# Performance work log

Hardware: AMD Instinct MI355X
Metric: run time of the kernel (lower is better)

## Reference

```python
import jax, jax.numpy as jnp
import numpy as np

N, E, T = 6144, 98304, 32
D_IN, D, D_FF, H, OUT = 128, 256, 256, 4, 2
DH = D // H
EPS = 1e-5


def setup_inputs() -> dict:
    key = jax.random.key(0)
    ks = jax.random.split(key, 24)
    s = 0.05
    inp = {
        "x": jax.random.normal(ks[0], (N, D_IN), jnp.float32),
        "edge_index": jax.random.randint(ks[1], (2, E), 0, N, jnp.int64 if jax.config.jax_enable_x64 else jnp.int32),
        "timesteps": jnp.sort(jax.random.randint(ks[2], (N,), 0, T)),
        "lin_l_w": jax.random.normal(ks[3], (D, D_IN), jnp.float32) * s,
        "lin_l_b": jnp.zeros((D,), jnp.float32),
        "lin_r_w": jax.random.normal(ks[4], (D, D_IN), jnp.float32) * s,
        "bn_gamma": jnp.ones((D,), jnp.float32),
        "bn_beta": jnp.zeros((D,), jnp.float32),
        "in_proj_w": jax.random.normal(ks[5], (2, 3 * D, D), jnp.float32) * s,
        "in_proj_b": jnp.zeros((2, 3 * D), jnp.float32),
        "out_w": jax.random.normal(ks[6], (2, D, D), jnp.float32) * s,
        "out_b": jnp.zeros((2, D), jnp.float32),
        "ff1_w": jax.random.normal(ks[7], (2, D_FF, D), jnp.float32) * s,
        "ff1_b": jnp.zeros((2, D_FF), jnp.float32),
        "ff2_w": jax.random.normal(ks[8], (2, D, D_FF), jnp.float32) * s,
        "ff2_b": jnp.zeros((2, D), jnp.float32),
        "ln1_g": jnp.ones((2, D), jnp.float32),
        "ln1_b": jnp.zeros((2, D), jnp.float32),
        "ln2_g": jnp.ones((2, D), jnp.float32),
        "ln2_b": jnp.zeros((2, D), jnp.float32),
        "cls_w": jax.random.normal(ks[9], (OUT, D), jnp.float32) * s,
        "cls_b": jnp.zeros((OUT,), jnp.float32),
    }
    return inp


def _layernorm(h, g, b):
    mu = jnp.mean(h, -1, keepdims=True)
    v = jnp.var(h, -1, keepdims=True)
    return (h - mu) * jax.lax.rsqrt(v + EPS) * g + b


def _forward(x, edge_index, timesteps, lin_l_w, lin_l_b, lin_r_w, bn_gamma, bn_beta,
             in_proj_w, in_proj_b, out_w, out_b, ff1_w, ff1_b, ff2_w, ff2_b,
             ln1_g, ln1_b, ln2_g, ln2_b, cls_w, cls_b):
    # SAGEConv (mean aggregation): out = lin_l(mean_{j->i} x_j) + lin_r(x_i)
    src, dst = edge_index[0], edge_index[1]
    agg = jax.ops.segment_sum(x[src], dst, num_segments=N)
    cnt = jax.ops.segment_sum(jnp.ones((E,), x.dtype), dst, num_segments=N)
    agg = agg / jnp.maximum(cnt, 1.0)[:, None]
    h = agg @ lin_l_w.T + lin_l_b + x @ lin_r_w.T

    # BatchNorm1d (training batch stats) + ReLU
    mu = jnp.mean(h, 0)
    var = jnp.var(h, 0)
    h = (h - mu) * jax.lax.rsqrt(var + EPS) * bn_gamma + bn_beta
    h = jax.nn.relu(h)

    # Per-timestep transformer == full attention with block-diagonal mask
    mask = timesteps[:, None] == timesteps[None, :]  # [N, N]
    neg = jnp.finfo(h.dtype).min

    for l in range(2):
        # self-attention (post-norm TransformerEncoderLayer)
        qkv = h @ in_proj_w[l].T + in_proj_b[l]             # [N, 3D]
        q, k, v = jnp.split(qkv, 3, axis=-1)
        q = q.reshape(N, H, DH).transpose(1, 0, 2)          # [H, N, DH]
        k = k.reshape(N, H, DH).transpose(1, 0, 2)
        v = v.reshape(N, H, DH).transpose(1, 0, 2)
        scores = jnp.einsum('hnd,hmd->hnm', q, k) / jnp.sqrt(jnp.asarray(DH, h.dtype))
        scores = jnp.where(mask[None], scores, neg)
        attn = jax.nn.softmax(scores, axis=-1)
        o = jnp.einsum('hnm,hmd->hnd', attn, v).transpose(1, 0, 2).reshape(N, D)
        o = o @ out_w[l].T + out_b[l]
        h = _layernorm(h + o, ln1_g[l], ln1_b[l])
        # FFN
        f = jax.nn.relu(h @ ff1_w[l].T + ff1_b[l]) @ ff2_w[l].T + ff2_b[l]
        h = _layernorm(h + f, ln2_g[l], ln2_b[l])

    return h @ cls_w.T + cls_b  # [N, OUT]


def reference(x, edge_index, timesteps, lin_l_w, lin_l_b, lin_r_w, bn_gamma, bn_beta,
              in_proj_w, in_proj_b, out_w, out_b, ff1_w, ff1_b, ff2_w, ff2_b,
              ln1_g, ln1_b, ln2_g, ln2_b, cls_w, cls_b):
    return _forward(x, edge_index, timesteps, lin_l_w, lin_l_b, lin_r_w, bn_gamma, bn_beta,
                    in_proj_w, in_proj_b, out_w, out_b, ff1_w, ff1_b, ff2_w, ff2_b,
                    ln1_g, ln1_b, ln2_g, ln2_b, cls_w, cls_b)
```

## Files before the change

kernel.cpp:

```cpp
#include <hip/hip_runtime.h>

#define NN   6144
#define EE   98304
#define DIN  128
#define DD   256
#define TT   32
#define NH   4
#define ATTN_Z 6
#define WROWS 3328

typedef __attribute__((ext_vector_type(8))) short short8;
typedef __attribute__((ext_vector_type(4))) float f32x4;
typedef unsigned short u16;

__device__ __forceinline__ float bf2f(u16 u) {
    return __uint_as_float(((unsigned)u) << 16);
}
__device__ __forceinline__ u16 f2bf(float f) {
    unsigned u = __float_as_uint(f);
    return (u16)((u + 0x7fffu + ((u >> 16) & 1u)) >> 16);
}
__device__ __forceinline__ unsigned pk2(float a, float b) {
    return (unsigned)f2bf(a) | ((unsigned)f2bf(b) << 16);
}
__device__ __forceinline__ float bnrelu(float v, float s, float q, float g, float b) {
    float mu = s * (1.0f / NN);
    float var = q * (1.0f / NN) - mu * mu;
    return fmaxf((v - mu) * rsqrtf(var + 1e-5f) * g + b, 0.0f);
}

__global__ void aml_hist_k(const int* __restrict__ ei, int* __restrict__ deg) {
    int e = blockIdx.x * 256 + threadIdx.x;
    if (e < EE) atomicAdd(&deg[ei[EE + e]], 1);
}

__global__ void aml_scan_k(const int* __restrict__ deg, int* __restrict__ rowptr,
                           int* __restrict__ cursor) {
    int t = threadIdx.x;
    int base = t * 24;
    int loc[24];
    int s = 0;
    #pragma unroll
    for (int j = 0; j < 24; ++j) { loc[j] = s; s += deg[base + j]; }
    __shared__ int part[256];
    part[t] = s;
    __syncthreads();
    for (int o = 1; o < 256; o <<= 1) {
        int v = (t >= o) ? part[t - o] : 0;
        __syncthreads();
        part[t] += v;
        __syncthreads();
    }
    int off = (t > 0) ? part[t - 1] : 0;
    #pragma unroll
    for (int j = 0; j < 24; ++j) {
        rowptr[base + j] = off + loc[j];
        cursor[base + j] = off + loc[j];
    }
    if (t == 255) rowptr[NN] = part[255];
}

__global__ void aml_scatter2_k(const int* __restrict__ ei, int* __restrict__ cursor,
                               int* __restrict__ eid) {
    int e = blockIdx.x * 256 + threadIdx.x;
    if (e >= EE) return;
    int slot = atomicAdd(&cursor[ei[EE + e]], 1);
    eid[slot] = ei[e];
}

__global__ void aml_gather_k(const float* __restrict__ x, const int* __restrict__ rowptr,
                             const int* __restrict__ eid, u16* __restrict__ ac) {
    int node = blockIdx.x * 4 + (threadIdx.x >> 6);
    int lane = threadIdx.x & 63;
    int p0 = rowptr[node], p1 = rowptr[node + 1];
    float ax = 0.f, ay = 0.f;
    int j = p0;
    for (; j + 1 < p1; j += 2) {
        int s0 = eid[j], s1 = eid[j + 1];
        float2 v0 = *(const float2*)(x + (size_t)s0 * DIN + lane * 2);
        float2 v1 = *(const float2*)(x + (size_t)s1 * DIN + lane * 2);
        ax += v0.x + v1.x; ay += v0.y + v1.y;
    }
    if (j < p1) {
        float2 v = *(const float2*)(x + (size_t)eid[j] * DIN + lane * 2);
        ax += v.x; ay += v.y;
    }
    float inv = 1.0f / fmaxf((float)(p1 - p0), 1.0f);
    float2 xr = *(const float2*)(x + (size_t)node * DIN + lane * 2);
    *(unsigned*)(ac + (size_t)node * DD + lane * 2) = pk2(ax * inv, ay * inv);
    *(unsigned*)(ac + (size_t)node * DD + DIN + lane * 2) = pk2(xr.x, xr.y);
}

__global__ void aml_prep_k(const float* __restrict__ lin_l_w, const float* __restrict__ lin_r_w,
                           const float* __restrict__ inp_w, const float* __restrict__ out_w,
                           const float* __restrict__ ff1_w, const float* __restrict__ ff2_w,
                           const int* __restrict__ ts, u16* __restrict__ wb,
                           int* __restrict__ offs, float* __restrict__ zero_region) {
    int r = blockIdx.x;
    if (r > WROWS) {
        zero_region[(r - WROWS - 1) * 256 + threadIdx.x] = 0.0f;
        return;
    }
    if (r == WROWS) {
        int t = threadIdx.x;
        if (t <= TT) {
            int lo = 0, hi = NN;
            while (lo < hi) { int mid = (lo + hi) >> 1; if (ts[mid] < t) lo = mid + 1; else hi = mid; }
            offs[t] = lo;
        }
        return;
    }
    int k = threadIdx.x;
    float v;
    if (r < 256) {
        v = (k < DIN) ? lin_l_w[r * DIN + k] : lin_r_w[r * DIN + (k - DIN)];
    } else {
        int r2 = r - 256;
        int l = r2 / 1536, r3 = r2 % 1536;
        const float* src; int rr;
        if (r3 < 768)       { src = inp_w + (size_t)l * 768 * DD; rr = r3; }
        else if (r3 < 1024) { src = out_w + (size_t)l * DD * DD;  rr = r3 - 768; }
        else if (r3 < 1280) { src = ff1_w + (size_t)l * DD * DD;  rr = r3 - 1024; }
        else                { src = ff2_w + (size_t)l * DD * DD;  rr = r3 - 1280; }
        v = src[(size_t)rr * DD + k];
    }
    wb[(size_t)r * DD + k] = f2bf(v);
}

template <int RELU, int AMODE, int CF32, int BNSTAT, int CT2>
__global__ __launch_bounds__(256)
void aml_gemm_k(const void* __restrict__ A, const u16* __restrict__ Wb,
                const float* __restrict__ bias, void* __restrict__ C, int M,
                float* __restrict__ stats, const float* __restrict__ bng,
                const float* __restrict__ bnb, float* __restrict__ h2) {
    __shared__ __align__(16) unsigned char lds[65536];
    const int t = threadIdx.x;
    const int brow = blockIdx.x * 64;
    const int bcol = blockIdx.y * (64 * CT2);

    #pragma unroll
    for (int p = 0; p < 8; ++p) {
        int c = t + p * 256;
        int row = c >> 5;
        int colb = (c & 31) * 16;
        int dst = row * 512 + (colb ^ ((row & 7) << 4));
        if (AMODE == 2) {
            int d0 = (c & 31) * 8;
            const u16* sA = (const u16*)A + (size_t)(brow + row) * 256 + d0;
            uint4 raw = *(const uint4*)sA;
            const u16* rp = (const u16*)&raw;
            float av[8];
            #pragma unroll
            for (int i = 0; i < 8; ++i) {
                int d = d0 + i;
                av[i] = bnrelu(bf2f(rp[i]), stats[d], stats[DD + d], bng[d], bnb[d]);
            }
            if (blockIdx.y == 0) {
                float* hp = h2 + (size_t)(brow + row) * 256 + d0;
                *(float4*)hp = make_float4(av[0], av[1], av[2], av[3]);
                *(float4*)(hp + 4) = make_float4(av[4], av[5], av[6], av[7]);
            }
            uint4 pa = { pk2(av[0], av[1]), pk2(av[2], av[3]), pk2(av[4], av[5]), pk2(av[6], av[7]) };
            *(uint4*)(lds + dst) = pa;
        } else {
            const u16* sA = (const u16*)A + (size_t)(brow + row) * 256 + (c & 31) * 8;
            *(uint4*)(lds + dst) = *(const uint4*)sA;
        }
        *(uint4*)(lds + 32768 + dst) =
            *(const uint4*)(Wb + (size_t)(bcol + row) * 256 + (c & 31) * 8);
    }
    __syncthreads();

    const int wave = t >> 6, lane = t & 63;
    const int lrow = lane & 15, lk = lane >> 4;
    const int arow = wave * 16 + lrow;

    short8 af[8];
    #pragma unroll
    for (int ks = 0; ks < 8; ++ks) {
        int kbyte = ks * 64 + lk * 16;
        af[ks] = *(const short8*)(lds + arow * 512 + (kbyte ^ ((arow & 7) << 4)));
    }

    f32x4 acc[CT2][4] = {};
    #pragma unroll
    for (int c2 = 0; c2 < CT2; ++c2) {
        if (c2) {
            __syncthreads();
            #pragma unroll
            for (int p = 0; p < 8; ++p) {
                int c = t + p * 256;
                int row = c >> 5;
                int colb = (c & 31) * 16;
                int dst = 32768 + row * 512 + (colb ^ ((row & 7) << 4));
                *(uint4*)(lds + dst) =
                    *(const uint4*)(Wb + (size_t)(bcol + c2 * 64 + row) * 256 + (c & 31) * 8);
            }
            __syncthreads();
        }
        #pragma unroll
        for (int ks = 0; ks < 8; ++ks) {
            int kbyte = ks * 64 + lk * 16;
            #pragma unroll
            for (int ct = 0; ct < 4; ++ct) {
                int wrow = ct * 16 + lrow;
                short8 bf = *(const short8*)(lds + 32768 + wrow * 512 + (kbyte ^ ((wrow & 7) << 4)));
                acc[c2][ct] = __builtin_amdgcn_mfma_f32_16x16x32_bf16(af[ks], bf, acc[c2][ct], 0, 0, 0);
            }
        }
    }

    #pragma unroll
    for (int c2 = 0; c2 < CT2; ++c2) {
        #pragma unroll
        for (int ct = 0; ct < 4; ++ct) {
            int col = bcol + c2 * 64 + ct * 16 + lrow;
            float bv = bias[col];
            float s = 0.f, q = 0.f;
            #pragma unroll
            for (int r = 0; r < 4; ++r) {
                int grow = brow + wave * 16 + lk * 4 + r;
                float v = acc[c2][ct][r] + bv;
                if (RELU) v = fmaxf(v, 0.0f);
                if (CF32) ((float*)C)[(size_t)grow * M + col] = v;
                else      ((u16*)C)[(size_t)grow * M + col] = f2bf(v);
                if (BNSTAT) { s += v; q += v * v; }
            }
            if (BNSTAT) {
                s += __shfl_xor(s, 16); s += __shfl_xor(s, 32);
                q += __shfl_xor(q, 16); q += __shfl_xor(q, 32);
                if (lk == 0) {
                    atomicAdd(&stats[col], s);
                    atomicAdd(&stats[DD + col], q);
                }
            }
        }
    }
}

#define TAIL_GEMM(WPTR, LOADA)                                                            \
    _Pragma("unroll")                                                                     \
    for (int kc = 0; kc < 4; ++kc) {                                                      \
        __syncthreads();                                                                  \
        _Pragma("unroll")                                                                 \
        for (int p = 0; p < 8; ++p) {                                                     \
            int c = t + p * 256;                                                          \
            int row = c >> 3, sub = c & 7;                                                \
            *(uint4*)(Wl + row * 128 + ((sub * 16) ^ ((row & 7) << 4))) =                 \
                *(const uint4*)((WPTR) + (size_t)row * 256 + kc * 64 + sub * 8);          \
        }                                                                                 \
        __syncthreads();                                                                  \
        if ((LOADA) && kc == 0) {                                                         \
            _Pragma("unroll")                                                             \
            for (int ks = 0; ks < 8; ++ks) {                                              \
                int kbyte = ks * 64 + lk * 16;                                            \
                af[ks] = *(const short8*)(Al + lrow * 512 + (kbyte ^ ((lrow & 7) << 4))); \
            }                                                                             \
        }                                                                                 \
        _Pragma("unroll")                                                                 \
        for (int s = 0; s < 2; ++s) {                                                     \
            int kb = s * 64 + lk * 16;                                                    \
            _Pragma("unroll")                                                             \
            for (int ct = 0; ct < 4; ++ct) {                                              \
                int wrow = wcol + ct * 16 + lrow;                                         \
                short8 bf = *(const short8*)(Wl + wrow * 128 + (kb ^ ((wrow & 7) << 4))); \
                acc[ct] = __builtin_amdgcn_mfma_f32_16x16x32_bf16(af[kc * 2 + s], bf,     \
                                                                  acc[ct], 0, 0, 0);      \
            }                                                                             \
        }                                                                                 \
    }

#define WRITE_AL(VARR)                                                                    \
    _Pragma("unroll")                                                                     \
    for (int ct = 0; ct < 4; ++ct) {                                                      \
        _Pragma("unroll")                                                                 \
        for (int r = 0; r < 4; ++r) {                                                     \
            int row = lk * 4 + r, col = wcol + ct * 16 + lrow;                            \
            *(u16*)(Al + row * 512 + ((col * 2) ^ ((row & 7) << 4))) = f2bf(VARR[ct][r]); \
        }                                                                                 \
    }

#define ROW_LN_STATS(S4, Q4, MU, IV)                                                      \
    _Pragma("unroll")                                                                     \
    for (int off = 1; off < 16; off <<= 1) {                                              \
        _Pragma("unroll")                                                                 \
        for (int r = 0; r < 4; ++r) {                                                     \
            S4[r] += __shfl_xor(S4[r], off);                                              \
            Q4[r] += __shfl_xor(Q4[r], off);                                              \
        }                                                                                 \
    }                                                                                     \
    if (lrow == 0) {                                                                      \
        _Pragma("unroll")                                                                 \
        for (int r = 0; r < 4; ++r) {                                                     \
            reds[wave][lk * 4 + r] = S4[r];                                               \
            redq[wave][lk * 4 + r] = Q4[r];                                               \
        }                                                                                 \
    }                                                                                     \
    __syncthreads();                                                                      \
    _Pragma("unroll")                                                                     \
    for (int r = 0; r < 4; ++r) {                                                         \
        int rr = lk * 4 + r;                                                              \
        float S = reds[0][rr] + reds[1][rr] + reds[2][rr] + reds[3][rr];                  \
        float Q = redq[0][rr] + redq[1][rr] + redq[2][rr] + redq[3][rr];                  \
        MU[r] = S * (1.0f / DD);                                                          \
        IV[r] = rsqrtf(Q * (1.0f / DD) - MU[r] * MU[r] + 1e-5f);                          \
    }

template <int LAST>
__global__ __launch_bounds__(256)
void aml_tail_k(const u16* __restrict__ A, float* __restrict__ h2,
                const u16* __restrict__ Wout, const float* __restrict__ bout,
                const float* __restrict__ g1, const float* __restrict__ b1,
                const u16* __restrict__ Wff1, const float* __restrict__ bff1,
                const u16* __restrict__ Wff2, const float* __restrict__ bff2,
                const float* __restrict__ g2, const float* __restrict__ b2,
                const u16* __restrict__ Wq, const float* __restrict__ bq,
                u16* __restrict__ qkv,
                const float* __restrict__ cls_w, const float* __restrict__ cls_b,
                float* __restrict__ out) {
    __shared__ __align__(16) unsigned char Al[8192];
    __shared__ __align__(16) unsigned char Wl[32768];
    __shared__ float reds[4][16], redq[4][16];
    __shared__ float redc[2][4][16];
    const int t = threadIdx.x;
    const int brow = blockIdx.x * 16;
    const int wave = t >> 6, lane = t & 63;
    const int lrow = lane & 15, lk = lane >> 4;
    const int wcol = wave * 64;

    #pragma unroll
    for (int p = 0; p < 2; ++p) {
        int c = t + p * 256;
        int row = c >> 5, c8 = c & 31;
        *(uint4*)(Al + row * 512 + ((c8 * 16) ^ ((row & 7) << 4))) =
            *(const uint4*)(A + (size_t)(brow + row) * 256 + c8 * 8);
    }

    short8 af[8];
    f32x4 acc[4];

    #pragma unroll
    for (int ct = 0; ct < 4; ++ct) acc[ct] = (f32x4){0.f, 0.f, 0.f, 0.f};
    TAIL_GEMM(Wout, true)

    float ln1v[4][4];
    {
        float s4[4] = {}, q4[4] = {};
        #pragma unroll
        for (int ct = 0; ct < 4; ++ct) {
            int col = wcol + ct * 16 + lrow;
            float bvv = bout[col];
            #pragma unroll
            for (int r = 0; r < 4; ++r) {
                int grow = brow + lk * 4 + r;
                float v = acc[ct][r] + bvv + h2[(size_t)grow * DD + col];
                acc[ct][r] = v;
                s4[r] += v; q4[r] += v * v;
            }
        }
        float mu[4], iv[4];
        ROW_LN_STATS(s4, q4, mu, iv)
        #pragma unroll
        for (int ct = 0; ct < 4; ++ct) {
            int col = wcol + ct * 16 + lrow;
            float gv = g1[col], bb = b1[col];
            #pragma unroll
            for (int r = 0; r < 4; ++r)
                ln1v[ct][r] = (acc[ct][r] - mu[r]) * iv[r] * gv + bb;
        }
        WRITE_AL(ln1v)
    }

    #pragma unroll
    for (int ct = 0; ct < 4; ++ct) acc[ct] = (f32x4){0.f, 0.f, 0.f, 0.f};
    TAIL_GEMM(Wff1, true)
    {
        float fv[4][4];
        #pragma unroll
        for (int ct = 0; ct < 4; ++ct) {
            int col = wcol + ct * 16 + lrow;
            float bvv = bff1[col];
            #pragma unroll
            for (int r = 0; r < 4; ++r)
                fv[ct][r] = fmaxf(acc[ct][r] + bvv, 0.0f);
        }
        __syncthreads();
        WRITE_AL(fv)
    }

    #pragma unroll
    for (int ct = 0; ct < 4; ++ct) acc[ct] = (f32x4){0.f, 0.f, 0.f, 0.f};
    TAIL_GEMM(Wff2, true)
    float ln2v[4][4];
    {
        float s4[4] = {}, q4[4] = {};
        #pragma unroll
        for (int ct = 0; ct < 4; ++ct) {
            int col = wcol + ct * 16 + lrow;
            float bvv = bff2[col];
            #pragma unroll
            for (int r = 0; r < 4; ++r) {
                float v = acc[ct][r] + bvv + ln1v[ct][r];
                acc[ct][r] = v;
                s4[r] += v; q4[r] += v * v;
            }
        }
        float mu[4], iv[4];
        ROW_LN_STATS(s4, q4, mu, iv)
        #pragma unroll
        for (int ct = 0; ct < 4; ++ct) {
            int col = wcol + ct * 16 + lrow;
            float gv = g2[col], bb = b2[col];
            #pragma unroll
            for (int r = 0; r < 4; ++r) {
                float v = (acc[ct][r] - mu[r]) * iv[r] * gv + bb;
                ln2v[ct][r] = v;
                if (!LAST) {
                    int grow = brow + lk * 4 + r;
                    h2[(size_t)grow * DD + col] = v;
                }
            }
        }
        if (!LAST) {
            WRITE_AL(ln2v)
        }
    }

    if (!LAST) {
        #pragma unroll
        for (int cg = 0; cg < 3; ++cg) {
            #pragma unroll
            for (int ct = 0; ct < 4; ++ct) acc[ct] = (f32x4){0.f, 0.f, 0.f, 0.f};
            TAIL_GEMM(Wq + (size_t)cg * 256 * 256, cg == 0)
            #pragma unroll
            for (int ct = 0; ct < 4; ++ct) {
                int col = cg * 256 + wcol + ct * 16 + lrow;
                float bvv = bq[col];
                #pragma unroll
                for (int r = 0; r < 4; ++r) {
                    int grow = brow + lk * 4 + r;
                    qkv[(size_t)grow * 768 + col] = f2bf(acc[ct][r] + bvv);
                }
            }
        }
    } else {
        float c0[4] = {}, c1[4] = {};
        #pragma unroll
        for (int ct = 0; ct < 4; ++ct) {
            int col = wcol + ct * 16 + lrow;
            float w0 = cls_w[col], w1 = cls_w[DD + col];
            #pragma unroll
            for (int r = 0; r < 4; ++r) {
                c0[r] += ln2v[ct][r] * w0;
                c1[r] += ln2v[ct][r] * w1;
            }
        }
        #pragma unroll
        for (int off = 1; off < 16; off <<= 1) {
            #pragma unroll
            for (int r = 0; r < 4; ++r) {
                c0[r] += __shfl_xor(c0[r], off);
                c1[r] += __shfl_xor(c1[r], off);
            }
        }
        if (lrow == 0) {
            #pragma unroll
            for (int r = 0; r < 4; ++r) {
                redc[0][wave][lk * 4 + r] = c0[r];
                redc[1][wave][lk * 4 + r] = c1[r];
            }
        }
        __syncthreads();
        if (wave == 0 && lrow == 0) {
            float cb0 = cls_b[0], cb1 = cls_b[1];
            #pragma unroll
            for (int r = 0; r < 4; ++r) {
                int rr = lk * 4 + r;
                float o0 = redc[0][0][rr] + redc[0][1][rr] + redc[0][2][rr] + redc[0][3][rr];
                float o1 = redc[1][0][rr] + redc[1][1][rr] + redc[1][2][rr] + redc[1][3][rr];
                out[(brow + rr) * 2]     = o0 + cb0;
                out[(brow + rr) * 2 + 1] = o1 + cb1;
            }
        }
    }
}

__global__ __launch_bounds__(256)
void aml_attn_k(const u16* __restrict__ qkv, const int* __restrict__ offs,
                u16* __restrict__ o) {
    int tb = blockIdx.x, head = blockIdx.y, z = blockIdx.z;
    int start = offs[tb], end = offs[tb + 1];
    int S = end - start;
    if (S <= z * 64) return;
    int t = threadIdx.x, wave = t >> 6, lane = t & 63;
    int lq = lane & 15, lk = lane >> 4;
    int qoff = head * 64;

    __shared__ __align__(16) unsigned char Kl[8192];
    __shared__ __align__(16) unsigned char Vt[8192];
    __shared__ __align__(16) unsigned char Pl[4][2048];
    __shared__ float Ol[4][16][65];

    int qi = start + z * 64 + wave * 16 + lq;
    int qic = min(qi, end - 1);
    const u16* qp = qkv + (size_t)qic * 768 + qoff + lk * 8;
    short8 qf[2];
    qf[0] = *(const short8*)qp;
    qf[1] = *(const short8*)(qp + 32);

    float m = -1e30f, l = 0.f;
    f32x4 acc[4] = {};

    int ntile = (S + 63) >> 6;
    for (int tile = 0; tile < ntile; ++tile) {
        int jcnt = S - tile * 64; if (jcnt > 64) jcnt = 64;
        {
            int j = t >> 2, d0 = (t & 3) * 16;
            unsigned char* krow = Kl + j * 128;
            if (j < jcnt) {
                const u16* kp = qkv + (size_t)(start + tile * 64 + j) * 768 + 256 + qoff + d0;
                *(uint4*)(krow + ((d0 * 2) ^ ((j & 7) << 4))) = *(const uint4*)kp;
                *(uint4*)(krow + ((d0 * 2 + 16) ^ ((j & 7) << 4))) = *(const uint4*)(kp + 8);
            } else {
                uint4 zz = { 0, 0, 0, 0 };
                *(uint4*)(krow + ((d0 * 2) ^ ((j & 7) << 4))) = zz;
                *(uint4*)(krow + ((d0 * 2 + 16) ^ ((j & 7) << 4))) = zz;
            }
        }
        {
            int j0 = (t & 31) * 2, d0v = (t >> 5) * 8;
            const u16* vbase = qkv + (size_t)(start + tile * 64) * 768 + 512 + qoff + d0v;
            uint4 va = { 0, 0, 0, 0 }, vb = { 0, 0, 0, 0 };
            if (j0 < jcnt)     va = *(const uint4*)(vbase + (size_t)j0 * 768);
            if (j0 + 1 < jcnt) vb = *(const uint4*)(vbase + (size_t)(j0 + 1) * 768);
            const u16* pa = (const u16*)&va;
            const u16* pb = (const u16*)&vb;
            #pragma unroll
            for (int i = 0; i < 8; ++i) {
                int d = d0v + i;
                unsigned w = (unsigned)pa[i] | ((unsigned)pb[i] << 16);
                *(unsigned*)(Vt + d * 128 + ((j0 * 2) ^ ((d & 7) << 4))) = w;
            }
        }
        __syncthreads();

        f32x4 sv[4];
        #pragma unroll
        for (int kt = 0; kt < 4; ++kt) {
            int kr = kt * 16 + lq;
            f32x4 s = {};
            #pragma unroll
            for (int ks = 0; ks < 2; ++ks) {
                short8 kf = *(const short8*)(Kl + kr * 128 + ((ks * 64 + lk * 16) ^ ((kr & 7) << 4)));
                s = __builtin_amdgcn_mfma_f32_16x16x32_bf16(kf, qf[ks], s, 0, 0, 0);
            }
            sv[kt] = s;
        }
        float pm = -1e30f;
        #pragma unroll
        for (int kt = 0; kt < 4; ++kt) {
            #pragma unroll
            for (int r = 0; r < 4; ++r) {
                int kk = tile * 64 + kt * 16 + lk * 4 + r;
                float s = (kk < S) ? sv[kt][r] * 0.125f : -1e30f;
                sv[kt][r] = s;
                pm = fmaxf(pm, s);
            }
        }
        pm = fmaxf(pm, __shfl_xor(pm, 16));
        pm = fmaxf(pm, __shfl_xor(pm, 32));
        float mn = fmaxf(m, pm);
        float corr = __expf(m - mn);
        m = mn;
        float ps = 0.f;
        #pragma unroll
        for (int kt = 0; kt < 4; ++kt) {
            #pragma unroll
            for (int r = 0; r < 4; ++r) {
                float p = __expf(sv[kt][r] - mn);
                sv[kt][r] = p;
                ps += p;
            }
            uint2 w = { pk2(sv[kt][0], sv[kt][1]), pk2(sv[kt][2], sv[kt][3]) };
            *(uint2*)(Pl[wave] + lq * 128 + ((kt * 32 + lk * 8) ^ ((lq & 7) << 4))) = w;
        }
        ps += __shfl_xor(ps, 16);
        ps += __shfl_xor(ps, 32);
        l = l * corr + ps;
        #pragma unroll
        for (int dt = 0; dt < 4; ++dt) {
            #pragma unroll
            for (int r = 0; r < 4; ++r) acc[dt][r] *= corr;
        }
        #pragma unroll
        for (int ks = 0; ks < 2; ++ks) {
            short8 pf = *(const short8*)(Pl[wave] + lq * 128 + ((ks * 64 + lk * 16) ^ ((lq & 7) << 4)));
            #pragma unroll
            for (int dt = 0; dt < 4; ++dt) {
                int dr = dt * 16 + lq;
                short8 vf = *(const short8*)(Vt + dr * 128 + ((ks * 64 + lk * 16) ^ ((dr & 7) << 4)));
                acc[dt] = __builtin_amdgcn_mfma_f32_16x16x32_bf16(vf, pf, acc[dt], 0, 0, 0);
            }
        }
        __syncthreads();
    }

    float linv = 1.0f / l;
    #pragma unroll
    for (int dt = 0; dt < 4; ++dt) {
        #pragma unroll
        for (int r = 0; r < 4; ++r)
            Ol[wave][lq][dt * 16 + lk * 4 + r] = acc[dt][r] * linv;
    }
    int q2 = lane >> 2, c2 = lane & 3;
    int qg = start + z * 64 + wave * 16 + q2;
    if (qg < end) {
        u16* op = o + (size_t)qg * DD + qoff + c2 * 16;
        const float* sp = &Ol[wave][q2][c2 * 16];
        #pragma unroll
        for (int i = 0; i < 8; ++i)
            ((unsigned*)op)[i] = pk2(sp[2 * i], sp[2 * i + 1]);
    }
}

extern "C" void kernel_launch(void* const* d_in, const int* in_sizes, int n_in,
                              void* d_out, int out_size, void* d_ws, size_t ws_size,
                              hipStream_t stream) {
    const float* x       = (const float*)d_in[0];
    const int*   ei      = (const int*)d_in[1];
    const int*   ts      = (const int*)d_in[2];
    const float* lin_l_w = (const float*)d_in[3];
    const float* lin_l_b = (const float*)d_in[4];
    const float* lin_r_w = (const float*)d_in[5];
    const float* bn_g    = (const float*)d_in[6];
    const float* bn_b    = (const float*)d_in[7];
    const float* inp_w   = (const float*)d_in[8];
    const float* inp_b   = (const float*)d_in[9];
    const float* out_w   = (const float*)d_in[10];
    const float* out_b   = (const float*)d_in[11];
    const float* ff1_w   = (const float*)d_in[12];
    const float* ff1_b   = (const float*)d_in[13];
    const float* ff2_w   = (const float*)d_in[14];
    const float* ff2_b   = (const float*)d_in[15];
    const float* ln1_g   = (const float*)d_in[16];
    const float* ln1_b   = (const float*)d_in[17];
    const float* ln2_g   = (const float*)d_in[18];
    const float* ln2_b   = (const float*)d_in[19];
    const float* cls_w   = (const float*)d_in[20];
    const float* cls_b   = (const float*)d_in[21];

    float* ws     = (float*)d_ws;
    float* stats  = ws;
    int*   deg    = (int*)(stats + 512);
    int*   rowptr = deg + NN;
    int*   cursor = rowptr + NN + 4;
    int*   eid    = cursor + NN;
    int*   offs   = eid + EE;
    u16*   wb     = (u16*)(offs + 64);
    u16*   hb     = wb + (size_t)WROWS * 256;
    float* h2     = (float*)(hb + (size_t)NN * DD);
    u16*   qkv    = (u16*)(h2 + (size_t)NN * DD);
    u16*   t1     = qkv + (size_t)NN * 768;
    u16*   ac     = qkv;

    const u16* wb_cat = wb;
    const u16* wb_inp[2] = { wb + (size_t)(256) * 256,        wb + (size_t)(256 + 1536) * 256 };
    const u16* wb_out[2] = { wb + (size_t)(256 + 768) * 256,  wb + (size_t)(256 + 1536 + 768) * 256 };
    const u16* wb_ff1[2] = { wb + (size_t)(256 + 1024) * 256, wb + (size_t)(256 + 1536 + 1024) * 256 };
    const u16* wb_ff2[2] = { wb + (size_t)(256 + 1280) * 256, wb + (size_t)(256 + 1536 + 1280) * 256 };

    aml_prep_k<<<WROWS + 27, 256, 0, stream>>>(lin_l_w, lin_r_w, inp_w, out_w, ff1_w, ff2_w,
                                               ts, wb, offs, stats);
    aml_hist_k<<<EE / 256, 256, 0, stream>>>(ei, deg);
    aml_scan_k<<<1, 256, 0, stream>>>(deg, rowptr, cursor);
    aml_scatter2_k<<<EE / 256, 256, 0, stream>>>(ei, cursor, eid);
    aml_gather_k<<<NN / 4, 256, 0, stream>>>(x, rowptr, eid, ac);
    aml_gemm_k<0, 0, 0, 1, 1><<<dim3(NN / 64, 4), 256, 0, stream>>>(
        ac, wb_cat, lin_l_b, hb, DD, stats, nullptr, nullptr, nullptr);
    aml_gemm_k<0, 2, 0, 0, 1><<<dim3(NN / 64, 12), 256, 0, stream>>>(
        hb, wb_inp[0], inp_b, qkv, 768, stats, bn_g, bn_b, h2);

    aml_attn_k<<<dim3(TT, NH, ATTN_Z), 256, 0, stream>>>(qkv, offs, t1);
    aml_tail_k<0><<<NN / 16, 256, 0, stream>>>(
        t1, h2, wb_out[0], out_b, ln1_g, ln1_b,
        wb_ff1[0], ff1_b, wb_ff2[0], ff2_b, ln2_g, ln2_b,
        wb_inp[1], inp_b + 768, qkv, nullptr, nullptr, nullptr);

    aml_attn_k<<<dim3(TT, NH, ATTN_Z), 256, 0, stream>>>(qkv, offs, t1);
    aml_tail_k<1><<<NN / 16, 256, 0, stream>>>(
        t1, h2, wb_out[1], out_b + DD, ln1_g + DD, ln1_b + DD,
        wb_ff1[1], ff1_b + DD, wb_ff2[1], ff2_b + DD, ln2_g + DD, ln2_b + DD,
        nullptr, nullptr, nullptr, cls_w, cls_b, (float*)d_out);
}
```

Measured before the change: 153.8 us.

## Split attention over key tiles with a separate log-sum-exp combine kernel

Each attention block now handles one 64-query by 64-key tile pair instead of looping over all key tiles. It writes unnormalized fp32 partial outputs plus per-row max and sum to workspace. A new combine kernel merges the partials per query with the usual rescaling and writes the bf16 output. The aim is more parallel blocks and shorter serial loops per block. The cost is extra fp32 partial traffic to global memory and one more launch per layer.

```diff
diff --git a/kernel.cpp b/kernel.cpp
--- a/kernel.cpp
+++ b/kernel.cpp
@@ -6,7 +6,8 @@
 #define DD   256
 #define TT   32
 #define NH   4
-#define ATTN_Z 6
+#define ZQ   6
+#define ZK   6
 #define WROWS 3328
 
 typedef __attribute__((ext_vector_type(8))) short short8;
@@ -487,11 +488,13 @@
 
 __global__ __launch_bounds__(256)
 void aml_attn_k(const u16* __restrict__ qkv, const int* __restrict__ offs,
-                u16* __restrict__ o) {
-    int tb = blockIdx.x, head = blockIdx.y, z = blockIdx.z;
+                float* __restrict__ Opart, float* __restrict__ mpart,
+                float* __restrict__ lpart) {
+    int tb = blockIdx.x, head = blockIdx.y;
+    int zq = blockIdx.z / ZK, zk = blockIdx.z % ZK;
     int start = offs[tb], end = offs[tb + 1];
     int S = end - start;
-    if (S <= z * 64) return;
+    if (S <= zq * 64 || zk * 64 >= S) return;
     int t = threadIdx.x, wave = t >> 6, lane = t & 63;
     int lq = lane & 15, lk = lane >> 4;
     int qoff = head * 64;
@@ -501,126 +504,147 @@
     __shared__ __align__(16) unsigned char Pl[4][2048];
     __shared__ float Ol[4][16][65];
 
-    int qi = start + z * 64 + wave * 16 + lq;
+    int qi = start + zq * 64 + wave * 16 + lq;
     int qic = min(qi, end - 1);
     const u16* qp = qkv + (size_t)qic * 768 + qoff + lk * 8;
     short8 qf[2];
     qf[0] = *(const short8*)qp;
     qf[1] = *(const short8*)(qp + 32);
 
-    float m = -1e30f, l = 0.f;
+    int jcnt = S - zk * 64; if (jcnt > 64) jcnt = 64;
+    {
+        int j = t >> 2, d0 = (t & 3) * 16;
+        unsigned char* krow = Kl + j * 128;
+        if (j < jcnt) {
+            const u16* kp = qkv + (size_t)(start + zk * 64 + j) * 768 + 256 + qoff + d0;
+            *(uint4*)(krow + ((d0 * 2) ^ ((j & 7) << 4))) = *(const uint4*)kp;
+            *(uint4*)(krow + ((d0 * 2 + 16) ^ ((j & 7) << 4))) = *(const uint4*)(kp + 8);
+        } else {
+            uint4 zz = { 0, 0, 0, 0 };
+            *(uint4*)(krow + ((d0 * 2) ^ ((j & 7) << 4))) = zz;
+            *(uint4*)(krow + ((d0 * 2 + 16) ^ ((j & 7) << 4))) = zz;
+        }
+    }
+    {
+        int j0 = (t & 31) * 2, d0v = (t >> 5) * 8;
+        const u16* vbase = qkv + (size_t)(start + zk * 64) * 768 + 512 + qoff + d0v;
+        uint4 va = { 0, 0, 0, 0 }, vb = { 0, 0, 0, 0 };
+        if (j0 < jcnt)     va = *(const uint4*)(vbase + (size_t)j0 * 768);
+        if (j0 + 1 < jcnt) vb = *(const uint4*)(vbase + (size_t)(j0 + 1) * 768);
+        const u16* pa = (const u16*)&va;
+        const u16* pb = (const u16*)&vb;
+        #pragma unroll
+        for (int i = 0; i < 8; ++i) {
+            int d = d0v + i;
+            unsigned w = (unsigned)pa[i] | ((unsigned)pb[i] << 16);
+            *(unsigned*)(Vt + d * 128 + ((j0 * 2) ^ ((d & 7) << 4))) = w;
+        }
+    }
+    __syncthreads();
+
+    f32x4 sv[4];
+    #pragma unroll
+    for (int kt = 0; kt < 4; ++kt) {
+        int kr = kt * 16 + lq;
+        f32x4 s = {};
+        #pragma unroll
+        for (int ks = 0; ks < 2; ++ks) {
+            short8 kf = *(const short8*)(Kl + kr * 128 + ((ks * 64 + lk * 16) ^ ((kr & 7) << 4)));
+            s = __builtin_amdgcn_mfma_f32_16x16x32_bf16(kf, qf[ks], s, 0, 0, 0);
+        }
+        sv[kt] = s;
+    }
+    float pm = -1e30f;
+    #pragma unroll
+    for (int kt = 0; kt < 4; ++kt) {
+        #pragma unroll
+        for (int r = 0; r < 4; ++r) {
+            int kk = zk * 64 + kt * 16 + lk * 4 + r;
+            float s = (kk < S) ? sv[kt][r] * 0.125f : -1e30f;
+            sv[kt][r] = s;
+            pm = fmaxf(pm, s);
+        }
+    }
+    pm = fmaxf(pm, __shfl_xor(pm, 16));
+    pm = fmaxf(pm, __shfl_xor(pm, 32));
+    float ps = 0.f;
+    #pragma unroll
+    for (int kt = 0; kt < 4; ++kt) {
+        #pragma unroll
+        for (int r = 0; r < 4; ++r) {
+            float p = __expf(sv[kt][r] - pm);
+            sv[kt][r] = p;
+            ps += p;
+        }
+        uint2 w = { pk2(sv[kt][0], sv[kt][1]), pk2(sv[kt][2], sv[kt][3]) };
+        *(uint2*)(Pl[wave] + lq * 128 + ((kt * 32 + lk * 8) ^ ((lq & 7) << 4))) = w;
+    }
+    ps += __shfl_xor(ps, 16);
+    ps += __shfl_xor(ps, 32);
+    if (lk == 0 && qi < end) {
+        mpart[((size_t)zk * NN + qi) * NH + head] = pm;
+        lpart[((size_t)zk * NN + qi) * NH + head] = ps;
+    }
     f32x4 acc[4] = {};
-
+    #pragma unroll
+    for (int ks = 0; ks < 2; ++ks) {
+        short8 pf = *(const short8*)(Pl[wave] + lq * 128 + ((ks * 64 + lk * 16) ^ ((lq & 7) << 4)));
+        #pragma unroll
+        for (int dt = 0; dt < 4; ++dt) {
+            int dr = dt * 16 + lq;
+            short8 vf = *(const short8*)(Vt + dr * 128 + ((ks * 64 + lk * 16) ^ ((dr & 7) << 4)));
+            acc[dt] = __builtin_amdgcn_mfma_f32_16x16x32_bf16(vf, pf, acc[dt], 0, 0, 0);
+        }
+    }
+
+    #pragma unroll
+    for (int dt = 0; dt < 4; ++dt) {
+        #pragma unroll
+        for (int r = 0; r < 4; ++r)
+            Ol[wave][lq][dt * 16 + lk * 4 + r] = acc[dt][r];
+    }
+    int q2 = lane >> 2, c2 = lane & 3;
+    int qg = start + zq * 64 + wave * 16 + q2;
+    if (qg < end) {
+        float* op = Opart + ((size_t)zk * NN + qg) * DD + qoff + c2 * 16;
+        const float* sp = &Ol[wave][q2][c2 * 16];
+        #pragma unroll
+        for (int i = 0; i < 4; ++i) ((float4*)op)[i] = *(const float4*)(sp + i * 4);
+    }
+}
+
+__global__ __launch_bounds__(256)
+void aml_comb_k(const float* __restrict__ Opart, const float* __restrict__ mpart,
+                const float* __restrict__ lpart, const int* __restrict__ ts,
+                const int* __restrict__ offs, u16* __restrict__ o) {
+    int t = threadIdx.x, head = t >> 6, lane = t & 63;
+    int lq = lane & 15, ld = lane >> 4;
+    int q = blockIdx.x * 16 + lq;
+    int tb = ts[q];
+    int S = offs[tb + 1] - offs[tb];
     int ntile = (S + 63) >> 6;
-    for (int tile = 0; tile < ntile; ++tile) {
-        int jcnt = S - tile * 64; if (jcnt > 64) jcnt = 64;
-        {
-            int j = t >> 2, d0 = (t & 3) * 16;
-            unsigned char* krow = Kl + j * 128;
-            if (j < jcnt) {
-                const u16* kp = qkv + (size_t)(start + tile * 64 + j) * 768 + 256 + qoff + d0;
-                *(uint4*)(krow + ((d0 * 2) ^ ((j & 7) << 4))) = *(const uint4*)kp;
-                *(uint4*)(krow + ((d0 * 2 + 16) ^ ((j & 7) << 4))) = *(const uint4*)(kp + 8);
-            } else {
-                uint4 zz = { 0, 0, 0, 0 };
-                *(uint4*)(krow + ((d0 * 2) ^ ((j & 7) << 4))) = zz;
-                *(uint4*)(krow + ((d0 * 2 + 16) ^ ((j & 7) << 4))) = zz;
-            }
-        }
-        {
-            int j0 = (t & 31) * 2, d0v = (t >> 5) * 8;
-            const u16* vbase = qkv + (size_t)(start + tile * 64) * 768 + 512 + qoff + d0v;
-            uint4 va = { 0, 0, 0, 0 }, vb = { 0, 0, 0, 0 };
-            if (j0 < jcnt)     va = *(const uint4*)(vbase + (size_t)j0 * 768);
-            if (j0 + 1 < jcnt) vb = *(const uint4*)(vbase + (size_t)(j0 + 1) * 768);
-            const u16* pa = (const u16*)&va;
-            const u16* pb = (const u16*)&vb;
-            #pragma unroll
-            for (int i = 0; i < 8; ++i) {
-                int d = d0v + i;
-                unsigned w = (unsigned)pa[i] | ((unsigned)pb[i] << 16);
-                *(unsigned*)(Vt + d * 128 + ((j0 * 2) ^ ((d & 7) << 4))) = w;
-            }
-        }
-        __syncthreads();
-
-        f32x4 sv[4];
-        #pragma unroll
-        for (int kt = 0; kt < 4; ++kt) {
-            int kr = kt * 16 + lq;
-            f32x4 s = {};
-            #pragma unroll
-            for (int ks = 0; ks < 2; ++ks) {
-                short8 kf = *(const short8*)(Kl + kr * 128 + ((ks * 64 + lk * 16) ^ ((kr & 7) << 4)));
-                s = __builtin_amdgcn_mfma_f32_16x16x32_bf16(kf, qf[ks], s, 0, 0, 0);
-            }
-            sv[kt] = s;
-        }
-        float pm = -1e30f;
-        #pragma unroll
-        for (int kt = 0; kt < 4; ++kt) {
-            #pragma unroll
-            for (int r = 0; r < 4; ++r) {
-                int kk = tile * 64 + kt * 16 + lk * 4 + r;
-                float s = (kk < S) ? sv[kt][r] * 0.125f : -1e30f;
-                sv[kt][r] = s;
-                pm = fmaxf(pm, s);
-            }
-        }
-        pm = fmaxf(pm, __shfl_xor(pm, 16));
-        pm = fmaxf(pm, __shfl_xor(pm, 32));
-        float mn = fmaxf(m, pm);
-        float corr = __expf(m - mn);
-        m = mn;
-        float ps = 0.f;
-        #pragma unroll
-        for (int kt = 0; kt < 4; ++kt) {
-            #pragma unroll
-            for (int r = 0; r < 4; ++r) {
-                float p = __expf(sv[kt][r] - mn);
-                sv[kt][r] = p;
-                ps += p;
-            }
-            uint2 w = { pk2(sv[kt][0], sv[kt][1]), pk2(sv[kt][2], sv[kt][3]) };
-            *(uint2*)(Pl[wave] + lq * 128 + ((kt * 32 + lk * 8) ^ ((lq & 7) << 4))) = w;
-        }
-        ps += __shfl_xor(ps, 16);
-        ps += __shfl_xor(ps, 32);
-        l = l * corr + ps;
-        #pragma unroll
-        for (int dt = 0; dt < 4; ++dt) {
-            #pragma unroll
-            for (int r = 0; r < 4; ++r) acc[dt][r] *= corr;
-        }
-        #pragma unroll
-        for (int ks = 0; ks < 2; ++ks) {
-            short8 pf = *(const short8*)(Pl[wave] + lq * 128 + ((ks * 64 + lk * 16) ^ ((lq & 7) << 4)));
-            #pragma unroll
-            for (int dt = 0; dt < 4; ++dt) {
-                int dr = dt * 16 + lq;
-                short8 vf = *(const short8*)(Vt + dr * 128 + ((ks * 64 + lk * 16) ^ ((dr & 7) << 4)));
-                acc[dt] = __builtin_amdgcn_mfma_f32_16x16x32_bf16(vf, pf, acc[dt], 0, 0, 0);
-            }
-        }
-        __syncthreads();
-    }
-
-    float linv = 1.0f / l;
-    #pragma unroll
-    for (int dt = 0; dt < 4; ++dt) {
-        #pragma unroll
-        for (int r = 0; r < 4; ++r)
-            Ol[wave][lq][dt * 16 + lk * 4 + r] = acc[dt][r] * linv;
-    }
-    int q2 = lane >> 2, c2 = lane & 3;
-    int qg = start + z * 64 + wave * 16 + q2;
-    if (qg < end) {
-        u16* op = o + (size_t)qg * DD + qoff + c2 * 16;
-        const float* sp = &Ol[wave][q2][c2 * 16];
-        #pragma unroll
-        for (int i = 0; i < 8; ++i)
-            ((unsigned*)op)[i] = pk2(sp[2 * i], sp[2 * i + 1]);
-    }
+
+    float M = -1e30f;
+    for (int i = 0; i < ntile; ++i)
+        M = fmaxf(M, mpart[((size_t)i * NN + q) * NH + head]);
+    float L = 0.f;
+    float ov[16] = {};
+    for (int i = 0; i < ntile; ++i) {
+        float w = __expf(mpart[((size_t)i * NN + q) * NH + head] - M);
+        L += lpart[((size_t)i * NN + q) * NH + head] * w;
+        const float* op = Opart + ((size_t)i * NN + q) * DD + head * 64 + ld * 16;
+        #pragma unroll
+        for (int j = 0; j < 16; j += 4) {
+            float4 v = *(const float4*)(op + j);
+            ov[j] += v.x * w; ov[j + 1] += v.y * w;
+            ov[j + 2] += v.z * w; ov[j + 3] += v.w * w;
+        }
+    }
+    float linv = 1.0f / L;
+    u16* dst = o + (size_t)q * DD + head * 64 + ld * 16;
+    #pragma unroll
+    for (int j = 0; j < 8; ++j)
+        ((unsigned*)dst)[j] = pk2(ov[2 * j] * linv, ov[2 * j + 1] * linv);
 }
 
 extern "C" void kernel_launch(void* const* d_in, const int* in_sizes, int n_in,
@@ -661,6 +685,9 @@
     float* h2     = (float*)(hb + (size_t)NN * DD);
     u16*   qkv    = (u16*)(h2 + (size_t)NN * DD);
     u16*   t1     = qkv + (size_t)NN * 768;
+    float* Opart  = (float*)(t1 + (size_t)NN * DD);
+    float* mpart  = Opart + (size_t)ZK * NN * DD;
+    float* lpart  = mpart + (size_t)ZK * NN * NH;
     u16*   ac     = qkv;
 
     const u16* wb_cat = wb;
@@ -680,13 +707,15 @@
     aml_gemm_k<0, 2, 0, 0, 1><<<dim3(NN / 64, 12), 256, 0, stream>>>(
         hb, wb_inp[0], inp_b, qkv, 768, stats, bn_g, bn_b, h2);
 
-    aml_attn_k<<<dim3(TT, NH, ATTN_Z), 256, 0, stream>>>(qkv, offs, t1);
+    aml_attn_k<<<dim3(TT, NH, ZQ * ZK), 256, 0, stream>>>(qkv, offs, Opart, mpart, lpart);
+    aml_comb_k<<<NN / 16, 256, 0, stream>>>(Opart, mpart, lpart, ts, offs, t1);
     aml_tail_k<0><<<NN / 16, 256, 0, stream>>>(
         t1, h2, wb_out[0], out_b, ln1_g, ln1_b,
         wb_ff1[0], ff1_b, wb_ff2[0], ff2_b, ln2_g, ln2_b,
         wb_inp[1], inp_b + 768, qkv, nullptr, nullptr, nullptr);
 
-    aml_attn_k<<<dim3(TT, NH, ATTN_Z), 256, 0, stream>>>(qkv, offs, t1);
+    aml_attn_k<<<dim3(TT, NH, ZQ * ZK), 256, 0, stream>>>(qkv, offs, Opart, mpart, lpart);
+    aml_comb_k<<<NN / 16, 256, 0, stream>>>(Opart, mpart, lpart, ts, offs, t1);
     aml_tail_k<1><<<NN / 16, 256, 0, stream>>>(
         t1, h2, wb_out[1], out_b + DD, ln1_g + DD, ln1_b + DD,
         wb_ff1[1], ff1_b + DD, wb_ff2[1], ff2_b + DD, ln2_g + DD, ln2_b + DD,
```

After: 181.1 us. 17.7% more time.
